# Performance work log

Hardware: AMD Instinct MI355X
Metric: run time of the kernel (lower is better)

## Reference

```python
import jax, jax.numpy as jnp
import numpy as np
import math

B, N, H = 2, 2048, 256
NUM_HEADS, HEAD_DIM = 8, 32
WIN = 32            # window_size
WIN_LEN = 2 * WIN + 1


def setup_inputs() -> dict:
    key = jax.random.key(0)
    ks = jax.random.split(key, 12)
    s = 0.02
    return {
        "x": jax.random.normal(ks[0], (B, N, 4, H), dtype=jnp.float32),
        "Wq": jax.random.normal(ks[1], (H, H), dtype=jnp.float32) * s,
        "bq": jnp.zeros((H,), jnp.float32),
        "Wk": jax.random.normal(ks[2], (H, H), dtype=jnp.float32) * s,
        "bk": jnp.zeros((H,), jnp.float32),
        "Wv": jax.random.normal(ks[3], (H, H), dtype=jnp.float32) * s,
        "bv": jnp.zeros((H,), jnp.float32),
        "Wo": jax.random.normal(ks[4], (H, 3 * H), dtype=jnp.float32) * s,
        "bo": jnp.zeros((3 * H,), jnp.float32),
        "Wvec": jax.random.normal(ks[5], (H, 2 * H), dtype=jnp.float32) * s,
        "alpha_dot": jnp.float32(1.0),
        "alpha_norm": jnp.float32(1.0),
        "Wg": jax.random.normal(ks[6], (2 * H, H), dtype=jnp.float32) * s,
        "bg": jnp.zeros((H,), jnp.float32),
    }


def reference(x, Wq, bq, Wk, bk, Wv, bv, Wo, bo, Wvec, alpha_dot, alpha_norm, Wg, bg):
    h, d = NUM_HEADS, HEAD_DIM
    scale = 1.0 / math.sqrt(d)

    x_scalar = x[:, :, 0]          # (B,N,H)
    vec = x[:, :, 1:4]             # (B,N,3,H)

    q = (x_scalar @ Wq + bq).reshape(B, N, h, d).transpose(0, 2, 1, 3)  # (B,h,N,d)
    k = (x_scalar @ Wk + bk).reshape(B, N, h, d).transpose(0, 2, 1, 3)
    v = (x_scalar @ Wv + bv).reshape(B, N, h, d).transpose(0, 2, 1, 3)

    vec_proj = vec @ Wvec                                # (B,N,3,2H)
    vec1, vec2 = vec_proj[..., :H], vec_proj[..., H:]
    vec_dot = (vec1 * vec2).sum(axis=-2)                 # (B,N,H)
    vec_norm = jnp.linalg.norm(vec, axis=2)              # (B,N,H)

    # (B,N,3,h,d) -> (B,h,N,3*d)
    vec_flat = vec.reshape(B, N, 3, h, d).transpose(0, 3, 1, 2, 4).reshape(B, h, N, 3 * d)

    # sliding-window attention via padded gather (matches torch unfold semantics)
    BH = B * h
    q_l = q.reshape(BH, N, d)
    k_l = k.reshape(BH, N, d)
    v_l = v.reshape(BH, N, d)
    vec_l = vec_flat.reshape(BH, N, 3 * d)

    pad = ((0, 0), (WIN, WIN), (0, 0))
    k_p = jnp.pad(k_l, pad)
    v_p = jnp.pad(v_l, pad)
    vec_p = jnp.pad(vec_l, pad)

    idx = jnp.arange(N)[:, None] + jnp.arange(WIN_LEN)[None, :]  # (N,WIN_LEN)
    k_win = k_p[:, idx]        # (BH,N,WIN_LEN,d)
    v_win = v_p[:, idx]
    vec_win = vec_p[:, idx]    # (BH,N,WIN_LEN,3d)

    attn_scores = jnp.einsum('bid,biwd->biw', q_l, k_win) * scale
    attn_weights = jax.nn.softmax(attn_scores, axis=-1)  # (BH,N,WIN_LEN)

    x_agg = jnp.einsum('biw,biwd->bid', attn_weights, v_win).reshape(B, h, N, d)
    vec_aggr = jnp.einsum('biw,biwd->bid', attn_weights, vec_win).reshape(B, h, N, 3 * d)

    x_out = x_agg.transpose(0, 2, 1, 3).reshape(B, N, H)
    vec_aggr = vec_aggr.reshape(B, h, N, 3, d).transpose(0, 2, 3, 1, 4).reshape(B, N, 3, H)

    invariants = jnp.concatenate([alpha_dot * vec_dot, alpha_norm * vec_norm], axis=-1)
    gate = jax.nn.sigmoid(invariants @ Wg + bg)[:, :, None, :]   # (B,N,1,H)
    vec_combined = gate * vec_aggr + vec                          # gated add mixing

    o = x_out @ Wo + bo
    o1, o2, o3 = o[..., :H], o[..., H:2 * H], o[..., 2 * H:]
    x_updated = vec_dot * o1 + vec_norm * o2 + o3

    x_final = jnp.concatenate([x_updated[:, :, None], vec_combined], axis=2)  # (B,N,4,H)
    return x_final, attn_weights
```

## Files before the change

kernel.cpp:

```cpp
#include <hip/hip_runtime.h>
#include <hip/hip_bf16.h>
#include <math.h>

#define Bc 2
#define Nn 2048
#define Hh 256
#define NH 8
#define Dd 32
#define WIN 32
#define WL 65
#define BN (Bc * Nn)

typedef __attribute__((ext_vector_type(8))) short bf16x8;
typedef __attribute__((ext_vector_type(4))) short s16x4;
typedef __attribute__((ext_vector_type(4))) float f32x4;

__device__ inline short f2bf(float f) {
    union { float f; unsigned u; } v; v.f = f;
    unsigned r = v.u + 0x7fffu + ((v.u >> 16) & 1u);
    return (short)(r >> 16);
}

__device__ inline bf16x8 cvt8(float4 a, float4 b) {
    union { __hip_bfloat162 h[4]; bf16x8 v; } u;
    u.h[0] = __float22bfloat162_rn(make_float2(a.x, a.y));
    u.h[1] = __float22bfloat162_rn(make_float2(a.z, a.w));
    u.h[2] = __float22bfloat162_rn(make_float2(b.x, b.y));
    u.h[3] = __float22bfloat162_rn(make_float2(b.z, b.w));
    return u.v;
}

__global__ __launch_bounds__(256) void prep_kernel(
    const float* __restrict__ x, const float* __restrict__ alpha_norm,
    const float* __restrict__ Wq, const float* __restrict__ Wk, const float* __restrict__ Wv,
    const float* __restrict__ Wvec, const float* __restrict__ Wg, const float* __restrict__ Wo,
    float* __restrict__ vec_norm, short* __restrict__ inv_bf,
    short* __restrict__ WqkvT, short* __restrict__ WvecT,
    short* __restrict__ WgT, short* __restrict__ WoT) {
    __shared__ float Ts[32][33];
    const int t = threadIdx.x;
    if (blockIdx.x >= 640) {
        const int gid = (blockIdx.x - 640) * 256 + t;
        const int bn = gid >> 6, c4 = gid & 63;
        const size_t base = (size_t)bn * 1024 + c4 * 4;
        const float4 v0 = *(const float4*)&x[base + 256];
        const float4 v1 = *(const float4*)&x[base + 512];
        const float4 v2 = *(const float4*)&x[base + 768];
        float4 nr;
        nr.x = sqrtf(v0.x * v0.x + v1.x * v1.x + v2.x * v2.x);
        nr.y = sqrtf(v0.y * v0.y + v1.y * v1.y + v2.y * v2.y);
        nr.z = sqrtf(v0.z * v0.z + v1.z * v1.z + v2.z * v2.z);
        nr.w = sqrtf(v0.w * v0.w + v1.w * v1.w + v2.w * v2.w);
        *(float4*)&vec_norm[(size_t)bn * 256 + c4 * 4] = nr;
        const float an = alpha_norm[0];
        s16x4 iv;
        iv[0] = f2bf(an * nr.x); iv[1] = f2bf(an * nr.y);
        iv[2] = f2bf(an * nr.z); iv[3] = f2bf(an * nr.w);
        *(s16x4*)&inv_bf[(size_t)bn * 512 + 256 + c4 * 4] = iv;
        return;
    }
    const int cc = t & 31, r0 = t >> 5;
    const int id = blockIdx.x;
    const float* W; int ldw; short* WT; int ldwt; int n0s, k0, n0d;
    if (id < 192) {
        const int tn = id >> 3, tk = id & 7, sel = tn >> 3;
        W = sel == 0 ? Wq : (sel == 1 ? Wk : Wv); ldw = 256;
        n0s = (tn & 7) * 32; k0 = tk * 32; WT = WqkvT; ldwt = 256; n0d = tn * 32;
    } else if (id < 320) {
        const int id2 = id - 192, tn = id2 >> 3, tk = id2 & 7;
        W = Wvec; ldw = 512; n0s = tn * 32; k0 = tk * 32; WT = WvecT; ldwt = 256; n0d = n0s;
    } else if (id < 448) {
        const int id3 = id - 320, tn = id3 >> 4, tk = id3 & 15;
        W = Wg; ldw = 256; n0s = tn * 32; k0 = tk * 32; WT = WgT; ldwt = 512; n0d = n0s;
    } else {
        const int id4 = id - 448, tn = id4 >> 3, tk = id4 & 7;
        W = Wo; ldw = 768; n0s = tn * 32; k0 = tk * 32; WT = WoT; ldwt = 256; n0d = n0s;
    }
#pragma unroll
    for (int p = 0; p < 4; ++p) {
        const int rr = r0 + p * 8;
        Ts[rr][cc] = W[(size_t)(k0 + rr) * ldw + n0s + cc];
    }
    __syncthreads();
#pragma unroll
    for (int p = 0; p < 4; ++p) {
        const int rr = r0 + p * 8;
        WT[(size_t)(n0d + rr) * ldwt + k0 + cc] = f2bf(Ts[cc][rr]);
    }
}

__global__ __launch_bounds__(256) void mid_kernel(
    const float* __restrict__ x,
    const short* __restrict__ WqkvT, const short* __restrict__ WvecT,
    const float* __restrict__ bq, const float* __restrict__ bk, const float* __restrict__ bv,
    const float* __restrict__ alpha_dot,
    short* __restrict__ Qb, short* __restrict__ Kb, short* __restrict__ Vb,
    float* __restrict__ vec_dot, short* __restrict__ inv_bf) {
    __shared__ __align__(16) short lds[10240];
    const int bid = blockIdx.x;
    const int t = threadIdx.x, lane = t & 63, wid = t >> 6;
    const int wm = wid & 1, wn = wid >> 1, quad = lane >> 4, lm = lane & 15;
    const int srow = t >> 2, scg = (t & 3) * 8;

    if (bid < 384) {
        short* As = lds;
        short* Bs = lds + 2560;
        const int row0 = (bid & 63) * 64, col0 = (bid >> 6) * 128;
        f32x4 acc[2][4];
#pragma unroll
        for (int mt = 0; mt < 2; ++mt)
#pragma unroll
            for (int nt = 0; nt < 4; ++nt) {
                f32x4 z = {0.f, 0.f, 0.f, 0.f};
                acc[mt][nt] = z;
            }
        float4 pa0 = *(const float4*)&x[(size_t)(row0 + srow) * 1024 + scg];
        float4 pa1 = *(const float4*)&x[(size_t)(row0 + srow) * 1024 + scg + 4];
        bf16x8 pb[2];
#pragma unroll
        for (int p = 0; p < 2; ++p) {
            const int idx = t + p * 256;
            pb[p] = *(const bf16x8*)&WqkvT[(size_t)(col0 + (idx >> 2)) * 256 + (idx & 3) * 8];
        }
        for (int k0 = 0; k0 < 256; k0 += 32) {
            *(bf16x8*)&As[srow * 40 + scg] = cvt8(pa0, pa1);
#pragma unroll
            for (int p = 0; p < 2; ++p) {
                const int idx = t + p * 256;
                *(bf16x8*)&Bs[(idx >> 2) * 40 + (idx & 3) * 8] = pb[p];
            }
            __syncthreads();
            if (k0 + 32 < 256) {
                pa0 = *(const float4*)&x[(size_t)(row0 + srow) * 1024 + k0 + 32 + scg];
                pa1 = *(const float4*)&x[(size_t)(row0 + srow) * 1024 + k0 + 32 + scg + 4];
#pragma unroll
                for (int p = 0; p < 2; ++p) {
                    const int idx = t + p * 256;
                    pb[p] = *(const bf16x8*)&WqkvT[(size_t)(col0 + (idx >> 2)) * 256 + k0 + 32 + (idx & 3) * 8];
                }
            }
            bf16x8 af[2], bfr[4];
#pragma unroll
            for (int mt = 0; mt < 2; ++mt)
                af[mt] = *(bf16x8*)&As[(wm * 32 + mt * 16 + lm) * 40 + quad * 8];
#pragma unroll
            for (int nt = 0; nt < 4; ++nt)
                bfr[nt] = *(bf16x8*)&Bs[(wn * 64 + nt * 16 + lm) * 40 + quad * 8];
#pragma unroll
            for (int mt = 0; mt < 2; ++mt)
#pragma unroll
                for (int nt = 0; nt < 4; ++nt)
                    acc[mt][nt] = __builtin_amdgcn_mfma_f32_16x16x32_bf16(
                        af[mt], bfr[nt], acc[mt][nt], 0, 0, 0);
            __syncthreads();
        }
        const int chunk = col0 >> 8;
        short* dst = chunk == 0 ? Qb : (chunk == 1 ? Kb : Vb);
        const float* bias = chunk == 0 ? bq : (chunk == 1 ? bk : bv);
#pragma unroll
        for (int mt = 0; mt < 2; ++mt)
#pragma unroll
            for (int nt = 0; nt < 4; ++nt) {
                const int cm = (col0 + wn * 64 + nt * 16 + lm) & 255;
                const float bb = bias[cm];
#pragma unroll
                for (int r = 0; r < 4; ++r) {
                    const int row = row0 + wm * 32 + mt * 16 + quad * 4 + r;
                    dst[(size_t)row * 256 + cm] = f2bf(acc[mt][nt][r] + bb);
                }
            }
        return;
    }

    short* As = lds;
    short* Bs = lds + 7680;
    const int vb = bid - 384;
    const int row0 = (vb >> 3) * 64, ch0 = (vb & 7) * 32;
    const int bh_ = t >> 7, bc = (t >> 2) & 31, bcg = (t & 3) * 8;
    f32x4 acc[3][2][2];
#pragma unroll
    for (int p = 0; p < 3; ++p)
#pragma unroll
        for (int h = 0; h < 2; ++h)
#pragma unroll
            for (int mt = 0; mt < 2; ++mt) {
                f32x4 z = {0.f, 0.f, 0.f, 0.f};
                acc[p][h][mt] = z;
            }
    float4 pa0[3], pa1[3];
#pragma unroll
    for (int p = 0; p < 3; ++p) {
        pa0[p] = *(const float4*)&x[(size_t)(row0 + srow) * 1024 + (1 + p) * 256 + scg];
        pa1[p] = *(const float4*)&x[(size_t)(row0 + srow) * 1024 + (1 + p) * 256 + scg + 4];
    }
    bf16x8 pb = *(const bf16x8*)&WvecT[(size_t)(bh_ * 256 + ch0 + bc) * 256 + bcg];
    for (int k0 = 0; k0 < 256; k0 += 32) {
#pragma unroll
        for (int p = 0; p < 3; ++p)
            *(bf16x8*)&As[p * 2560 + srow * 40 + scg] = cvt8(pa0[p], pa1[p]);
        *(bf16x8*)&Bs[bh_ * 1280 + bc * 40 + bcg] = pb;
        __syncthreads();
        if (k0 + 32 < 256) {
#pragma unroll
            for (int p = 0; p < 3; ++p) {
                pa0[p] = *(const float4*)&x[(size_t)(row0 + srow) * 1024 + (1 + p) * 256 + k0 + 32 + scg];
                pa1[p] = *(const float4*)&x[(size_t)(row0 + srow) * 1024 + (1 + p) * 256 + k0 + 32 + scg + 4];
            }
            pb = *(const bf16x8*)&WvecT[(size_t)(bh_ * 256 + ch0 + bc) * 256 + k0 + 32 + bcg];
        }
        bf16x8 af[3][2], bfr[2];
#pragma unroll
        for (int p = 0; p < 3; ++p)
#pragma unroll
            for (int mt = 0; mt < 2; ++mt)
                af[p][mt] = *(bf16x8*)&As[p * 2560 + (wm * 32 + mt * 16 + lm) * 40 + quad * 8];
#pragma unroll
        for (int h = 0; h < 2; ++h)
            bfr[h] = *(bf16x8*)&Bs[h * 1280 + (wn * 16 + lm) * 40 + quad * 8];
#pragma unroll
        for (int p = 0; p < 3; ++p)
#pragma unroll
            for (int h = 0; h < 2; ++h)
#pragma unroll
                for (int mt = 0; mt < 2; ++mt)
                    acc[p][h][mt] = __builtin_amdgcn_mfma_f32_16x16x32_bf16(
                        af[p][mt], bfr[h], acc[p][h][mt], 0, 0, 0);
        __syncthreads();
    }
    const float ad = alpha_dot[0];
#pragma unroll
    for (int mt = 0; mt < 2; ++mt) {
        const int col = ch0 + wn * 16 + lm;
#pragma unroll
        for (int r = 0; r < 4; ++r) {
            const int row = row0 + wm * 32 + mt * 16 + quad * 4 + r;
            float dot = 0.f;
#pragma unroll
            for (int p = 0; p < 3; ++p)
                dot = fmaf(acc[p][0][mt][r], acc[p][1][mt][r], dot);
            vec_dot[(size_t)row * 256 + col] = dot;
            inv_bf[(size_t)row * 512 + col] = f2bf(ad * dot);
        }
    }
}

__global__ __launch_bounds__(256) void gate_attn_kernel(
    const short* __restrict__ inv_bf, const short* __restrict__ WgT,
    const float* __restrict__ bg,
    const short* __restrict__ Qb, const short* __restrict__ Kb,
    const short* __restrict__ Vb, const float* __restrict__ x,
    float* __restrict__ gate, float* __restrict__ attnw,
    float* __restrict__ vec_aggr, short* __restrict__ xout_bf) {
    __shared__ __align__(16) short lds[21760];
    const int bid = blockIdx.x;
    const int t = threadIdx.x, lane = t & 63, wid = t >> 6;
    const int wm = wid & 1, wn = wid >> 1, quad = lane >> 4, lm = lane & 15;

    if (bid < 256) {
        short* As = lds;
        short* Bs = lds + 2560;
        const int row0 = (bid & 63) * 64, col0 = (bid >> 6) * 64;
        const int srow = t >> 2, scg = (t & 3) * 8;
        f32x4 acc[2][2];
#pragma unroll
        for (int mt = 0; mt < 2; ++mt)
#pragma unroll
            for (int nt = 0; nt < 2; ++nt) {
                f32x4 z = {0.f, 0.f, 0.f, 0.f};
                acc[mt][nt] = z;
            }
        bf16x8 pa = *(const bf16x8*)&inv_bf[(size_t)(row0 + srow) * 512 + scg];
        bf16x8 pb = *(const bf16x8*)&WgT[(size_t)(col0 + srow) * 512 + scg];
        for (int k0 = 0; k0 < 512; k0 += 32) {
            *(bf16x8*)&As[srow * 40 + scg] = pa;
            *(bf16x8*)&Bs[srow * 40 + scg] = pb;
            __syncthreads();
            if (k0 + 32 < 512) {
                pa = *(const bf16x8*)&inv_bf[(size_t)(row0 + srow) * 512 + k0 + 32 + scg];
                pb = *(const bf16x8*)&WgT[(size_t)(col0 + srow) * 512 + k0 + 32 + scg];
            }
            bf16x8 af[2], bfr[2];
#pragma unroll
            for (int mt = 0; mt < 2; ++mt)
                af[mt] = *(bf16x8*)&As[(wm * 32 + mt * 16 + lm) * 40 + quad * 8];
#pragma unroll
            for (int nt = 0; nt < 2; ++nt)
                bfr[nt] = *(bf16x8*)&Bs[(wn * 32 + nt * 16 + lm) * 40 + quad * 8];
#pragma unroll
            for (int mt = 0; mt < 2; ++mt)
#pragma unroll
                for (int nt = 0; nt < 2; ++nt)
                    acc[mt][nt] = __builtin_amdgcn_mfma_f32_16x16x32_bf16(
                        af[mt], bfr[nt], acc[mt][nt], 0, 0, 0);
            __syncthreads();
        }
#pragma unroll
        for (int mt = 0; mt < 2; ++mt)
#pragma unroll
            for (int nt = 0; nt < 2; ++nt) {
                const int col = col0 + wn * 32 + nt * 16 + lm;
                const float bb = bg[col];
#pragma unroll
                for (int r = 0; r < 4; ++r) {
                    const int row = row0 + wm * 32 + mt * 16 + quad * 4 + r;
                    const float z = acc[mt][nt][r] + bb;
                    gate[(size_t)row * 256 + col] = 1.f / (1.f + __expf(-z));
                }
            }
        return;
    }

    short* Qs = lds;
    short* Ks = lds + 1280;
    short* Pb = lds + 5120;
    short* St = lds + 8448;
    const int ab = bid - 256;
    const int bh = ab >> 6, tile = ab & 63;
    const int b = bh >> 3, hd = bh & 7;
    const int i0 = tile * 32;

    for (int idx = t; idx < 32 * 104 / 2; idx += 256) ((int*)Pb)[idx] = 0;
    if (t < 128) {
        const int row = t >> 2, cg = t & 3;
        *(bf16x8*)&Qs[row * 40 + cg * 8] =
            *(const bf16x8*)&Qb[((size_t)(b * Nn + i0 + row)) * 256 + hd * 32 + cg * 8];
    }
#pragma unroll
    for (int kk = 0; kk < 2; ++kk) {
        const int idx = t + kk * 256;
        if (idx < 384) {
            const int row = idx >> 2, cg = idx & 3;
            const int j = i0 - WIN + row;
            bf16x8 kv = {0, 0, 0, 0, 0, 0, 0, 0};
            if (j >= 0 && j < Nn)
                kv = *(const bf16x8*)&Kb[((size_t)(b * Nn + j)) * 256 + hd * 32 + cg * 8];
            *(bf16x8*)&Ks[row * 40 + cg * 8] = kv;
        }
    }
    __syncthreads();

    if (wid < 2) {
        const int il0 = wid * 16;
        const bf16x8 aq = *(bf16x8*)&Qs[(il0 + lm) * 40 + quad * 8];
        f32x4 c[6];
#pragma unroll
        for (int nt = 0; nt < 6; ++nt) {
            const bf16x8 bk = *(bf16x8*)&Ks[(nt * 16 + lm) * 40 + quad * 8];
            f32x4 z = {0.f, 0.f, 0.f, 0.f};
            c[nt] = __builtin_amdgcn_mfma_f32_16x16x32_bf16(aq, bk, z, 0, 0, 0);
        }
        float mx[4] = {-1e30f, -1e30f, -1e30f, -1e30f};
#pragma unroll
        for (int nt = 0; nt < 6; ++nt)
#pragma unroll
            for (int r = 0; r < 4; ++r) {
                const int il = il0 + quad * 4 + r;
                const int w = nt * 16 + lm - il;
                const float v = (w >= 0 && w <= 64)
                    ? c[nt][r] * 0.17677669529663687f : -1e30f;
                c[nt][r] = v;
                mx[r] = fmaxf(mx[r], v);
            }
#pragma unroll
        for (int off = 1; off < 16; off <<= 1)
#pragma unroll
            for (int r = 0; r < 4; ++r) mx[r] = fmaxf(mx[r], __shfl_xor(mx[r], off, 64));
        float sm[4] = {0.f, 0.f, 0.f, 0.f};
#pragma unroll
        for (int nt = 0; nt < 6; ++nt)
#pragma unroll
            for (int r = 0; r < 4; ++r) {
                const int il = il0 + quad * 4 + r;
                const int w = nt * 16 + lm - il;
                const float e = (w >= 0 && w <= 64) ? __expf(c[nt][r] - mx[r]) : 0.f;
                c[nt][r] = e;
                sm[r] += e;
            }
#pragma unroll
        for (int off = 1; off < 16; off <<= 1)
#pragma unroll
            for (int r = 0; r < 4; ++r) sm[r] += __shfl_xor(sm[r], off, 64);
        float inv[4];
#pragma unroll
        for (int r = 0; r < 4; ++r) inv[r] = 1.f / sm[r];
#pragma unroll
        for (int nt = 0; nt < 6; ++nt)
#pragma unroll
            for (int r = 0; r < 4; ++r) {
                const int il = il0 + quad * 4 + r;
                const int jr = nt * 16 + lm;
                const int w = jr - il;
                if (w >= 0 && w <= 64) {
                    const float pw = c[nt][r] * inv[r];
                    attnw[((size_t)bh * Nn + (i0 + il)) * WL + w] = pw;
                    Pb[il * 104 + jr] = f2bf(pw);
                }
            }
    } else {
        const int tt = t - 128;
        const int chunk = tt >> 3, j0 = tt & 7;
#pragma unroll
        for (int it = 0; it < 12; ++it) {
            const int jr = j0 + it * 8;
            const int j = i0 - WIN + jr;
            bf16x8 val = {0, 0, 0, 0, 0, 0, 0, 0};
            if (j >= 0 && j < Nn) {
                if (chunk < 4) {
                    val = *(const bf16x8*)&Vb[((size_t)(b * Nn + j)) * 256 + hd * 32 + chunk * 8];
                } else {
                    const int vc = (chunk - 4) >> 2, d0 = ((chunk - 4) & 3) * 8;
                    const float* src = &x[((size_t)(b * Nn + j)) * 1024 + (1 + vc) * 256 + hd * 32 + d0];
                    val = cvt8(*(const float4*)src, *(const float4*)(src + 4));
                }
            }
#pragma unroll
            for (int u = 0; u < 8; ++u) St[(chunk * 8 + u) * 104 + jr] = val[u];
        }
    }
    __syncthreads();

    f32x4 acc[4];
#pragma unroll
    for (int nt = 0; nt < 4; ++nt) {
        f32x4 z = {0.f, 0.f, 0.f, 0.f};
        acc[nt] = z;
    }
#pragma unroll
    for (int ks = 0; ks < 3; ++ks) {
        const bf16x8 ap = *(bf16x8*)&Pb[(wm * 16 + lm) * 104 + ks * 32 + quad * 8];
#pragma unroll
        for (int nt = 0; nt < 4; ++nt) {
            const bf16x8 bs = *(bf16x8*)&St[(wn * 64 + nt * 16 + lm) * 104 + ks * 32 + quad * 8];
            acc[nt] = __builtin_amdgcn_mfma_f32_16x16x32_bf16(ap, bs, acc[nt], 0, 0, 0);
        }
    }
#pragma unroll
    for (int nt = 0; nt < 4; ++nt) {
        const int dim = wn * 64 + nt * 16 + lm;
#pragma unroll
        for (int r = 0; r < 4; ++r) {
            const int i = wm * 16 + quad * 4 + r;
            const size_t bn = (size_t)(b * Nn + i0 + i);
            if (dim < 32) {
                xout_bf[bn * 256 + hd * 32 + dim] = f2bf(acc[nt][r]);
            } else {
                const int dm = dim - 32, c = dm >> 5, dd = dm & 31;
                vec_aggr[((size_t)c * BN + bn) * 256 + hd * 32 + dd] = acc[nt][r];
            }
        }
    }
}

__global__ __launch_bounds__(256) void out_kernel(
    const short* __restrict__ A, const short* __restrict__ BT,
    const float* __restrict__ bo,
    const float* __restrict__ vec_dot, const float* __restrict__ vec_norm,
    const float* __restrict__ gate, const float* __restrict__ vec_aggr,
    const float* __restrict__ x, float* __restrict__ out) {
    __shared__ short As[64 * 40];
    __shared__ short Bs[3][64 * 40];
    const int row0 = (blockIdx.x & 63) * 64, ch0 = (blockIdx.x >> 6) * 64;
    const int t = threadIdx.x, lane = t & 63, wid = t >> 6;
    const int wm = wid & 1, wn = wid >> 1, quad = lane >> 4, lm = lane & 15;
    const int srow = t >> 2, scg = (t & 3) * 8;
    f32x4 acc[3][2][2];
#pragma unroll
    for (int p = 0; p < 3; ++p)
#pragma unroll
        for (int mt = 0; mt < 2; ++mt)
#pragma unroll
            for (int nt = 0; nt < 2; ++nt) {
                f32x4 z = {0.f, 0.f, 0.f, 0.f};
                acc[p][mt][nt] = z;
            }
    bf16x8 pa, pb[3];
    pa = *(const bf16x8*)&A[(size_t)(row0 + srow) * 256 + scg];
#pragma unroll
    for (int p = 0; p < 3; ++p)
        pb[p] = *(const bf16x8*)&BT[(size_t)(p * 256 + ch0 + srow) * 256 + scg];
    for (int k0 = 0; k0 < 256; k0 += 32) {
        *(bf16x8*)&As[srow * 40 + scg] = pa;
#pragma unroll
        for (int p = 0; p < 3; ++p)
            *(bf16x8*)&Bs[p][srow * 40 + scg] = pb[p];
        __syncthreads();
        if (k0 + 32 < 256) {
            pa = *(const bf16x8*)&A[(size_t)(row0 + srow) * 256 + k0 + 32 + scg];
#pragma unroll
            for (int p = 0; p < 3; ++p)
                pb[p] = *(const bf16x8*)&BT[(size_t)(p * 256 + ch0 + srow) * 256 + k0 + 32 + scg];
        }
        bf16x8 af[2], bfr[3][2];
#pragma unroll
        for (int mt = 0; mt < 2; ++mt)
            af[mt] = *(bf16x8*)&As[(wm * 32 + mt * 16 + lm) * 40 + quad * 8];
#pragma unroll
        for (int p = 0; p < 3; ++p)
#pragma unroll
            for (int nt = 0; nt < 2; ++nt)
                bfr[p][nt] = *(bf16x8*)&Bs[p][(wn * 32 + nt * 16 + lm) * 40 + quad * 8];
#pragma unroll
        for (int p = 0; p < 3; ++p)
#pragma unroll
            for (int mt = 0; mt < 2; ++mt)
#pragma unroll
                for (int nt = 0; nt < 2; ++nt)
                    acc[p][mt][nt] = __builtin_amdgcn_mfma_f32_16x16x32_bf16(
                        af[mt], bfr[p][nt], acc[p][mt][nt], 0, 0, 0);
        __syncthreads();
    }
#pragma unroll
    for (int mt = 0; mt < 2; ++mt)
#pragma unroll
        for (int nt = 0; nt < 2; ++nt) {
            const int col = ch0 + wn * 32 + nt * 16 + lm;
            const float b1 = bo[col], b2 = bo[256 + col], b3 = bo[512 + col];
#pragma unroll
            for (int r = 0; r < 4; ++r) {
                const int row = row0 + wm * 32 + mt * 16 + quad * 4 + r;
                const float o1 = acc[0][mt][nt][r] + b1;
                const float o2 = acc[1][mt][nt][r] + b2;
                const float o3 = acc[2][mt][nt][r] + b3;
                const float vd = vec_dot[(size_t)row * 256 + col];
                const float vn = vec_norm[(size_t)row * 256 + col];
                out[(size_t)row * 1024 + col] = vd * o1 + vn * o2 + o3;
            }
        }
#pragma unroll
    for (int c = 0; c < 3; ++c) {
#pragma unroll
        for (int it = 0; it < 4; ++it) {
            const int idx = t + it * 256;
            const int row = row0 + (idx >> 4), col = ch0 + (idx & 15) * 4;
            const float4 g4 = *(const float4*)&gate[(size_t)row * 256 + col];
            const float4 va = *(const float4*)&vec_aggr[((size_t)c * BN + row) * 256 + col];
            const float4 xv = *(const float4*)&x[(size_t)row * 1024 + (1 + c) * 256 + col];
            float4 o;
            o.x = fmaf(g4.x, va.x, xv.x);
            o.y = fmaf(g4.y, va.y, xv.y);
            o.z = fmaf(g4.z, va.z, xv.z);
            o.w = fmaf(g4.w, va.w, xv.w);
            *(float4*)&out[(size_t)row * 1024 + (1 + c) * 256 + col] = o;
        }
    }
}

extern "C" void kernel_launch(void* const* d_in, const int* in_sizes, int n_in,
                              void* d_out, int out_size, void* d_ws, size_t ws_size,
                              hipStream_t stream) {
    const float* x  = (const float*)d_in[0];
    const float* Wq = (const float*)d_in[1];
    const float* bq = (const float*)d_in[2];
    const float* Wk = (const float*)d_in[3];
    const float* bk = (const float*)d_in[4];
    const float* Wv = (const float*)d_in[5];
    const float* bv = (const float*)d_in[6];
    const float* Wo = (const float*)d_in[7];
    const float* bo = (const float*)d_in[8];
    const float* Wvec = (const float*)d_in[9];
    const float* alpha_dot  = (const float*)d_in[10];
    const float* alpha_norm = (const float*)d_in[11];
    const float* Wg = (const float*)d_in[12];
    const float* bg = (const float*)d_in[13];

    float* ws = (float*)d_ws;
    float* vec_dot  = ws;
    float* vec_norm = ws + 1048576;
    float* gate     = ws + 2097152;
    float* vec_aggr = ws + 3145728;
    short* sb = (short*)(ws + 6291456);
    short* xout_bf = sb;
    short* Q_bf    = sb + 1048576;
    short* K_bf    = sb + 2097152;
    short* V_bf    = sb + 3145728;
    short* inv_bf  = sb + 4194304;
    short* WqkvT   = sb + 6291456;
    short* WvecT   = sb + 6488064;
    short* WgT     = sb + 6619136;
    short* WoT     = sb + 6750208;

    float* out = (float*)d_out;
    float* attnw = out + (size_t)Bc * Nn * 4 * Hh;

    prep_kernel<<<1664, 256, 0, stream>>>(x, alpha_norm, Wq, Wk, Wv, Wvec, Wg, Wo,
                                          vec_norm, inv_bf, WqkvT, WvecT, WgT, WoT);
    mid_kernel<<<896, 256, 0, stream>>>(x, WqkvT, WvecT, bq, bk, bv, alpha_dot,
                                        Q_bf, K_bf, V_bf, vec_dot, inv_bf);
    gate_attn_kernel<<<1280, 256, 0, stream>>>(inv_bf, WgT, bg, Q_bf, K_bf, V_bf, x,
                                               gate, attnw, vec_aggr, xout_bf);
    out_kernel<<<256, 256, 0, stream>>>(xout_bf, WoT, bo, vec_dot, vec_norm,
                                        gate, vec_aggr, x, out);
}
```

Baseline: 157.4 us.

## Pre-cast x to bf16 once, store vec_aggr in bf16, retile vec-proj and out GEMMs

A first pass converts the scalar and vector channels of x to bf16 buffers, and those are reused by the QKV GEMM, the Wvec GEMM and the attention gather instead of re-reading and converting fp32 x each time. The intermediate vec_aggr is stored as bf16 to halve its write and read traffic. The Wvec GEMM is retiled to 16-row blocks that keep all three vector components and the full K dimension in LDS, and out_kernel uses 32-row tiles to launch twice as many blocks. The cost is an extra elementwise pass with more bf16 writes, a larger LDS footprint, and bf16 rounding of vec_aggr before the gated add.

```diff
diff --git a/kernel.cpp b/kernel.cpp
--- a/kernel.cpp
+++ b/kernel.cpp
@@ -20,7 +20,11 @@
     unsigned r = v.u + 0x7fffu + ((v.u >> 16) & 1u);
     return (short)(r >> 16);
 }
-
+__device__ inline float bf2f(short s) {
+    union { float f; unsigned u; } v;
+    v.u = ((unsigned)(unsigned short)s) << 16;
+    return v.f;
+}
 __device__ inline bf16x8 cvt8(float4 a, float4 b) {
     union { __hip_bfloat162 h[4]; bf16x8 v; } u;
     u.h[0] = __float22bfloat162_rn(make_float2(a.x, a.y));
@@ -30,37 +34,33 @@
     return u.v;
 }
 
-__global__ __launch_bounds__(256) void prep_kernel(
+__global__ __launch_bounds__(256) void castxw_kernel(
     const float* __restrict__ x, const float* __restrict__ alpha_norm,
     const float* __restrict__ Wq, const float* __restrict__ Wk, const float* __restrict__ Wv,
     const float* __restrict__ Wvec, const float* __restrict__ Wg, const float* __restrict__ Wo,
+    short* __restrict__ xs_bf, short* __restrict__ vec_bf,
     float* __restrict__ vec_norm, short* __restrict__ inv_bf,
     short* __restrict__ WqkvT, short* __restrict__ WvecT,
     short* __restrict__ WgT, short* __restrict__ WoT) {
     __shared__ float Ts[32][33];
+    if (blockIdx.x < 4096) {
+        const int idx = blockIdx.x * 256 + threadIdx.x;
+        const int bn = idx >> 8, ch = idx & 255;
+        const size_t base = (size_t)bn * 1024 + ch;
+        const float xs = x[base];
+        const float v0 = x[base + 256], v1 = x[base + 512], v2 = x[base + 768];
+        xs_bf[(size_t)bn * 256 + ch] = f2bf(xs);
+        vec_bf[((size_t)0 * BN + bn) * 256 + ch] = f2bf(v0);
+        vec_bf[((size_t)1 * BN + bn) * 256 + ch] = f2bf(v1);
+        vec_bf[((size_t)2 * BN + bn) * 256 + ch] = f2bf(v2);
+        const float nrm = sqrtf(v0 * v0 + v1 * v1 + v2 * v2);
+        vec_norm[(size_t)bn * 256 + ch] = nrm;
+        inv_bf[(size_t)bn * 512 + 256 + ch] = f2bf(alpha_norm[0] * nrm);
+        return;
+    }
     const int t = threadIdx.x;
-    if (blockIdx.x >= 640) {
-        const int gid = (blockIdx.x - 640) * 256 + t;
-        const int bn = gid >> 6, c4 = gid & 63;
-        const size_t base = (size_t)bn * 1024 + c4 * 4;
-        const float4 v0 = *(const float4*)&x[base + 256];
-        const float4 v1 = *(const float4*)&x[base + 512];
-        const float4 v2 = *(const float4*)&x[base + 768];
-        float4 nr;
-        nr.x = sqrtf(v0.x * v0.x + v1.x * v1.x + v2.x * v2.x);
-        nr.y = sqrtf(v0.y * v0.y + v1.y * v1.y + v2.y * v2.y);
-        nr.z = sqrtf(v0.z * v0.z + v1.z * v1.z + v2.z * v2.z);
-        nr.w = sqrtf(v0.w * v0.w + v1.w * v1.w + v2.w * v2.w);
-        *(float4*)&vec_norm[(size_t)bn * 256 + c4 * 4] = nr;
-        const float an = alpha_norm[0];
-        s16x4 iv;
-        iv[0] = f2bf(an * nr.x); iv[1] = f2bf(an * nr.y);
-        iv[2] = f2bf(an * nr.z); iv[3] = f2bf(an * nr.w);
-        *(s16x4*)&inv_bf[(size_t)bn * 512 + 256 + c4 * 4] = iv;
-        return;
-    }
     const int cc = t & 31, r0 = t >> 5;
-    const int id = blockIdx.x;
+    const int id = blockIdx.x - 4096;
     const float* W; int ldw; short* WT; int ldwt; int n0s, k0, n0d;
     if (id < 192) {
         const int tn = id >> 3, tk = id & 7, sel = tn >> 3;
@@ -89,23 +89,24 @@
     }
 }
 
-__global__ __launch_bounds__(256) void mid_kernel(
-    const float* __restrict__ x,
+__global__ __launch_bounds__(256) void fused_mid(
+    const short* __restrict__ xs_bf, const short* __restrict__ vec_bf,
     const short* __restrict__ WqkvT, const short* __restrict__ WvecT,
     const float* __restrict__ bq, const float* __restrict__ bk, const float* __restrict__ bv,
     const float* __restrict__ alpha_dot,
     short* __restrict__ Qb, short* __restrict__ Kb, short* __restrict__ Vb,
     float* __restrict__ vec_dot, short* __restrict__ inv_bf) {
-    __shared__ __align__(16) short lds[10240];
+    __shared__ __align__(16) short lds[22912];
     const int bid = blockIdx.x;
     const int t = threadIdx.x, lane = t & 63, wid = t >> 6;
-    const int wm = wid & 1, wn = wid >> 1, quad = lane >> 4, lm = lane & 15;
-    const int srow = t >> 2, scg = (t & 3) * 8;
+    const int quad = lane >> 4, lm = lane & 15;
 
     if (bid < 384) {
         short* As = lds;
         short* Bs = lds + 2560;
         const int row0 = (bid & 63) * 64, col0 = (bid >> 6) * 128;
+        const int wm = wid & 1, wn = wid >> 1;
+        const int srow = t >> 2, scg = (t & 3) * 8;
         f32x4 acc[2][4];
 #pragma unroll
         for (int mt = 0; mt < 2; ++mt)
@@ -114,8 +115,7 @@
                 f32x4 z = {0.f, 0.f, 0.f, 0.f};
                 acc[mt][nt] = z;
             }
-        float4 pa0 = *(const float4*)&x[(size_t)(row0 + srow) * 1024 + scg];
-        float4 pa1 = *(const float4*)&x[(size_t)(row0 + srow) * 1024 + scg + 4];
+        bf16x8 pa = *(const bf16x8*)&xs_bf[(size_t)(row0 + srow) * 256 + scg];
         bf16x8 pb[2];
 #pragma unroll
         for (int p = 0; p < 2; ++p) {
@@ -123,7 +123,7 @@
             pb[p] = *(const bf16x8*)&WqkvT[(size_t)(col0 + (idx >> 2)) * 256 + (idx & 3) * 8];
         }
         for (int k0 = 0; k0 < 256; k0 += 32) {
-            *(bf16x8*)&As[srow * 40 + scg] = cvt8(pa0, pa1);
+            *(bf16x8*)&As[srow * 40 + scg] = pa;
 #pragma unroll
             for (int p = 0; p < 2; ++p) {
                 const int idx = t + p * 256;
@@ -131,8 +131,7 @@
             }
             __syncthreads();
             if (k0 + 32 < 256) {
-                pa0 = *(const float4*)&x[(size_t)(row0 + srow) * 1024 + k0 + 32 + scg];
-                pa1 = *(const float4*)&x[(size_t)(row0 + srow) * 1024 + k0 + 32 + scg + 4];
+                pa = *(const bf16x8*)&xs_bf[(size_t)(row0 + srow) * 256 + k0 + 32 + scg];
 #pragma unroll
                 for (int p = 0; p < 2; ++p) {
                     const int idx = t + p * 256;
@@ -173,71 +172,81 @@
     }
 
     short* As = lds;
-    short* Bs = lds + 7680;
+    short* Bs = lds + 12672;
     const int vb = bid - 384;
-    const int row0 = (vb >> 3) * 64, ch0 = (vb & 7) * 32;
-    const int bh_ = t >> 7, bc = (t >> 2) & 31, bcg = (t & 3) * 8;
+    const int row0 = (vb >> 1) * 16, ch0 = (vb & 1) * 128;
+
+#pragma unroll
+    for (int q = 0; q < 6; ++q) {
+        const int idx = t + q * 256;
+        const int p = idx >> 9, rem = idx & 511, row = rem >> 5, kg = rem & 31;
+        *(bf16x8*)&As[(p * 16 + row) * 264 + kg * 8] =
+            *(const bf16x8*)&vec_bf[((size_t)p * BN + row0 + row) * 256 + kg * 8];
+    }
     f32x4 acc[3][2][2];
 #pragma unroll
     for (int p = 0; p < 3; ++p)
 #pragma unroll
         for (int h = 0; h < 2; ++h)
 #pragma unroll
-            for (int mt = 0; mt < 2; ++mt) {
+            for (int nt = 0; nt < 2; ++nt) {
                 f32x4 z = {0.f, 0.f, 0.f, 0.f};
-                acc[p][h][mt] = z;
-            }
-    float4 pa0[3], pa1[3];
-#pragma unroll
-    for (int p = 0; p < 3; ++p) {
-        pa0[p] = *(const float4*)&x[(size_t)(row0 + srow) * 1024 + (1 + p) * 256 + scg];
-        pa1[p] = *(const float4*)&x[(size_t)(row0 + srow) * 1024 + (1 + p) * 256 + scg + 4];
-    }
-    bf16x8 pb = *(const bf16x8*)&WvecT[(size_t)(bh_ * 256 + ch0 + bc) * 256 + bcg];
+                acc[p][h][nt] = z;
+            }
+    bf16x8 pb[4];
+#pragma unroll
+    for (int q = 0; q < 4; ++q) {
+        const int idx = t + q * 256;
+        const int h = idx >> 9, rem = idx & 511, c = rem >> 2, kg = rem & 3;
+        pb[q] = *(const bf16x8*)&WvecT[(size_t)(h * 256 + ch0 + c) * 256 + kg * 8];
+    }
+    __syncthreads();
     for (int k0 = 0; k0 < 256; k0 += 32) {
 #pragma unroll
-        for (int p = 0; p < 3; ++p)
-            *(bf16x8*)&As[p * 2560 + srow * 40 + scg] = cvt8(pa0[p], pa1[p]);
-        *(bf16x8*)&Bs[bh_ * 1280 + bc * 40 + bcg] = pb;
+        for (int q = 0; q < 4; ++q) {
+            const int idx = t + q * 256;
+            const int h = idx >> 9, rem = idx & 511, c = rem >> 2, kg = rem & 3;
+            *(bf16x8*)&Bs[(h * 128 + c) * 40 + kg * 8] = pb[q];
+        }
         __syncthreads();
         if (k0 + 32 < 256) {
 #pragma unroll
-            for (int p = 0; p < 3; ++p) {
-                pa0[p] = *(const float4*)&x[(size_t)(row0 + srow) * 1024 + (1 + p) * 256 + k0 + 32 + scg];
-                pa1[p] = *(const float4*)&x[(size_t)(row0 + srow) * 1024 + (1 + p) * 256 + k0 + 32 + scg + 4];
-            }
-            pb = *(const bf16x8*)&WvecT[(size_t)(bh_ * 256 + ch0 + bc) * 256 + k0 + 32 + bcg];
-        }
-        bf16x8 af[3][2], bfr[2];
+            for (int q = 0; q < 4; ++q) {
+                const int idx = t + q * 256;
+                const int h = idx >> 9, rem = idx & 511, c = rem >> 2, kg = rem & 3;
+                pb[q] = *(const bf16x8*)&WvecT[(size_t)(h * 256 + ch0 + c) * 256 + k0 + 32 + kg * 8];
+            }
+        }
+        bf16x8 af[3], bfr[2][2];
 #pragma unroll
         for (int p = 0; p < 3; ++p)
-#pragma unroll
-            for (int mt = 0; mt < 2; ++mt)
-                af[p][mt] = *(bf16x8*)&As[p * 2560 + (wm * 32 + mt * 16 + lm) * 40 + quad * 8];
+            af[p] = *(bf16x8*)&As[(p * 16 + lm) * 264 + k0 + quad * 8];
 #pragma unroll
         for (int h = 0; h < 2; ++h)
-            bfr[h] = *(bf16x8*)&Bs[h * 1280 + (wn * 16 + lm) * 40 + quad * 8];
+#pragma unroll
+            for (int nt = 0; nt < 2; ++nt)
+                bfr[h][nt] = *(bf16x8*)&Bs[(h * 128 + wid * 32 + nt * 16 + lm) * 40 + quad * 8];
 #pragma unroll
         for (int p = 0; p < 3; ++p)
 #pragma unroll
             for (int h = 0; h < 2; ++h)
 #pragma unroll
-                for (int mt = 0; mt < 2; ++mt)
-                    acc[p][h][mt] = __builtin_amdgcn_mfma_f32_16x16x32_bf16(
-                        af[p][mt], bfr[h], acc[p][h][mt], 0, 0, 0);
+                for (int nt = 0; nt < 2; ++nt)
+                    acc[p][h][nt] = __builtin_amdgcn_mfma_f32_16x16x32_bf16(
+                        af[p], bfr[h][nt], acc[p][h][nt], 0, 0, 0);
         __syncthreads();
     }
     const float ad = alpha_dot[0];
 #pragma unroll
-    for (int mt = 0; mt < 2; ++mt) {
-        const int col = ch0 + wn * 16 + lm;
+    for (int nt = 0; nt < 2; ++nt) {
+        const int col = ch0 + wid * 32 + nt * 16 + lm;
 #pragma unroll
         for (int r = 0; r < 4; ++r) {
-            const int row = row0 + wm * 32 + mt * 16 + quad * 4 + r;
+            const int row = row0 + quad * 4 + r;
             float dot = 0.f;
 #pragma unroll
             for (int p = 0; p < 3; ++p)
-                dot = fmaf(acc[p][0][mt][r], acc[p][1][mt][r], dot);
+                dot = fmaf(acc[p][0][nt][r], acc[p][1][nt][r], dot);
             vec_dot[(size_t)row * 256 + col] = dot;
             inv_bf[(size_t)row * 512 + col] = f2bf(ad * dot);
         }
@@ -248,9 +257,9 @@
     const short* __restrict__ inv_bf, const short* __restrict__ WgT,
     const float* __restrict__ bg,
     const short* __restrict__ Qb, const short* __restrict__ Kb,
-    const short* __restrict__ Vb, const float* __restrict__ x,
+    const short* __restrict__ Vb, const short* __restrict__ vec_bf,
     float* __restrict__ gate, float* __restrict__ attnw,
-    float* __restrict__ vec_aggr, short* __restrict__ xout_bf) {
+    short* __restrict__ vec_aggr_bf, short* __restrict__ xout_bf) {
     __shared__ __align__(16) short lds[21760];
     const int bid = blockIdx.x;
     const int t = threadIdx.x, lane = t & 63, wid = t >> 6;
@@ -409,8 +418,7 @@
                     val = *(const bf16x8*)&Vb[((size_t)(b * Nn + j)) * 256 + hd * 32 + chunk * 8];
                 } else {
                     const int vc = (chunk - 4) >> 2, d0 = ((chunk - 4) & 3) * 8;
-                    const float* src = &x[((size_t)(b * Nn + j)) * 1024 + (1 + vc) * 256 + hd * 32 + d0];
-                    val = cvt8(*(const float4*)src, *(const float4*)(src + 4));
+                    val = *(const bf16x8*)&vec_bf[((size_t)vc * BN + b * Nn + j) * 256 + hd * 32 + d0];
                 }
             }
 #pragma unroll
@@ -445,7 +453,7 @@
                 xout_bf[bn * 256 + hd * 32 + dim] = f2bf(acc[nt][r]);
             } else {
                 const int dm = dim - 32, c = dm >> 5, dd = dm & 31;
-                vec_aggr[((size_t)c * BN + bn) * 256 + hd * 32 + dd] = acc[nt][r];
+                vec_aggr_bf[((size_t)c * BN + bn) * 256 + hd * 32 + dd] = f2bf(acc[nt][r]);
             }
         }
     }
@@ -455,45 +463,51 @@
     const short* __restrict__ A, const short* __restrict__ BT,
     const float* __restrict__ bo,
     const float* __restrict__ vec_dot, const float* __restrict__ vec_norm,
-    const float* __restrict__ gate, const float* __restrict__ vec_aggr,
+    const float* __restrict__ gate, const short* __restrict__ vec_aggr_bf,
     const float* __restrict__ x, float* __restrict__ out) {
-    __shared__ short As[64 * 40];
-    __shared__ short Bs[3][64 * 40];
-    const int row0 = (blockIdx.x & 63) * 64, ch0 = (blockIdx.x >> 6) * 64;
+    __shared__ __align__(16) short As[32 * 40];
+    __shared__ __align__(16) short Bs[3][64 * 40];
+    const int row0 = (blockIdx.x & 127) * 32, ch0 = (blockIdx.x >> 7) * 64;
     const int t = threadIdx.x, lane = t & 63, wid = t >> 6;
     const int wm = wid & 1, wn = wid >> 1, quad = lane >> 4, lm = lane & 15;
-    const int srow = t >> 2, scg = (t & 3) * 8;
-    f32x4 acc[3][2][2];
+    f32x4 acc[3][2];
 #pragma unroll
     for (int p = 0; p < 3; ++p)
 #pragma unroll
-        for (int mt = 0; mt < 2; ++mt)
-#pragma unroll
-            for (int nt = 0; nt < 2; ++nt) {
-                f32x4 z = {0.f, 0.f, 0.f, 0.f};
-                acc[p][mt][nt] = z;
-            }
-    bf16x8 pa, pb[3];
-    pa = *(const bf16x8*)&A[(size_t)(row0 + srow) * 256 + scg];
-#pragma unroll
-    for (int p = 0; p < 3; ++p)
-        pb[p] = *(const bf16x8*)&BT[(size_t)(p * 256 + ch0 + srow) * 256 + scg];
+        for (int nt = 0; nt < 2; ++nt) {
+            f32x4 z = {0.f, 0.f, 0.f, 0.f};
+            acc[p][nt] = z;
+        }
+    bf16x8 pa = {0, 0, 0, 0, 0, 0, 0, 0};
+    const int arow = t >> 2, acg = (t & 3) * 8;
+    if (t < 128) pa = *(const bf16x8*)&A[(size_t)(row0 + arow) * 256 + acg];
+    bf16x8 pb[3];
+#pragma unroll
+    for (int q = 0; q < 3; ++q) {
+        const int idx = t + q * 256;
+        const int p = idx >> 8, rem = idx & 255, brow = rem >> 2, bkg = (rem & 3) * 8;
+        pb[q] = *(const bf16x8*)&BT[(size_t)(p * 256 + ch0 + brow) * 256 + bkg];
+    }
     for (int k0 = 0; k0 < 256; k0 += 32) {
-        *(bf16x8*)&As[srow * 40 + scg] = pa;
-#pragma unroll
-        for (int p = 0; p < 3; ++p)
-            *(bf16x8*)&Bs[p][srow * 40 + scg] = pb[p];
+        if (t < 128) *(bf16x8*)&As[arow * 40 + acg] = pa;
+#pragma unroll
+        for (int q = 0; q < 3; ++q) {
+            const int idx = t + q * 256;
+            const int p = idx >> 8, rem = idx & 255, brow = rem >> 2, bkg = (rem & 3) * 8;
+            *(bf16x8*)&Bs[p][brow * 40 + bkg] = pb[q];
+        }
         __syncthreads();
         if (k0 + 32 < 256) {
-            pa = *(const bf16x8*)&A[(size_t)(row0 + srow) * 256 + k0 + 32 + scg];
-#pragma unroll
-            for (int p = 0; p < 3; ++p)
-                pb[p] = *(const bf16x8*)&BT[(size_t)(p * 256 + ch0 + srow) * 256 + k0 + 32 + scg];
-        }
-        bf16x8 af[2], bfr[3][2];
-#pragma unroll
-        for (int mt = 0; mt < 2; ++mt)
-            af[mt] = *(bf16x8*)&As[(wm * 32 + mt * 16 + lm) * 40 + quad * 8];
+            if (t < 128) pa = *(const bf16x8*)&A[(size_t)(row0 + arow) * 256 + k0 + 32 + acg];
+#pragma unroll
+            for (int q = 0; q < 3; ++q) {
+                const int idx = t + q * 256;
+                const int p = idx >> 8, rem = idx & 255, brow = rem >> 2, bkg = (rem & 3) * 8;
+                pb[q] = *(const bf16x8*)&BT[(size_t)(p * 256 + ch0 + brow) * 256 + k0 + 32 + bkg];
+            }
+        }
+        const bf16x8 af = *(bf16x8*)&As[(wm * 16 + lm) * 40 + quad * 8];
+        bf16x8 bfr[3][2];
 #pragma unroll
         for (int p = 0; p < 3; ++p)
 #pragma unroll
@@ -502,44 +516,40 @@
 #pragma unroll
         for (int p = 0; p < 3; ++p)
 #pragma unroll
-            for (int mt = 0; mt < 2; ++mt)
-#pragma unroll
-                for (int nt = 0; nt < 2; ++nt)
-                    acc[p][mt][nt] = __builtin_amdgcn_mfma_f32_16x16x32_bf16(
-                        af[mt], bfr[p][nt], acc[p][mt][nt], 0, 0, 0);
+            for (int nt = 0; nt < 2; ++nt)
+                acc[p][nt] = __builtin_amdgcn_mfma_f32_16x16x32_bf16(
+                    af, bfr[p][nt], acc[p][nt], 0, 0, 0);
         __syncthreads();
     }
 #pragma unroll
-    for (int mt = 0; mt < 2; ++mt)
-#pragma unroll
-        for (int nt = 0; nt < 2; ++nt) {
-            const int col = ch0 + wn * 32 + nt * 16 + lm;
-            const float b1 = bo[col], b2 = bo[256 + col], b3 = bo[512 + col];
-#pragma unroll
-            for (int r = 0; r < 4; ++r) {
-                const int row = row0 + wm * 32 + mt * 16 + quad * 4 + r;
-                const float o1 = acc[0][mt][nt][r] + b1;
-                const float o2 = acc[1][mt][nt][r] + b2;
-                const float o3 = acc[2][mt][nt][r] + b3;
-                const float vd = vec_dot[(size_t)row * 256 + col];
-                const float vn = vec_norm[(size_t)row * 256 + col];
-                out[(size_t)row * 1024 + col] = vd * o1 + vn * o2 + o3;
-            }
-        }
+    for (int nt = 0; nt < 2; ++nt) {
+        const int col = ch0 + wn * 32 + nt * 16 + lm;
+        const float b1 = bo[col], b2 = bo[256 + col], b3 = bo[512 + col];
+#pragma unroll
+        for (int r = 0; r < 4; ++r) {
+            const int row = row0 + wm * 16 + quad * 4 + r;
+            const float o1 = acc[0][nt][r] + b1;
+            const float o2 = acc[1][nt][r] + b2;
+            const float o3 = acc[2][nt][r] + b3;
+            const float vd = vec_dot[(size_t)row * 256 + col];
+            const float vn = vec_norm[(size_t)row * 256 + col];
+            out[(size_t)row * 1024 + col] = vd * o1 + vn * o2 + o3;
+        }
+    }
 #pragma unroll
     for (int c = 0; c < 3; ++c) {
 #pragma unroll
-        for (int it = 0; it < 4; ++it) {
+        for (int it = 0; it < 2; ++it) {
             const int idx = t + it * 256;
             const int row = row0 + (idx >> 4), col = ch0 + (idx & 15) * 4;
             const float4 g4 = *(const float4*)&gate[(size_t)row * 256 + col];
-            const float4 va = *(const float4*)&vec_aggr[((size_t)c * BN + row) * 256 + col];
+            const s16x4 va = *(const s16x4*)&vec_aggr_bf[((size_t)c * BN + row) * 256 + col];
             const float4 xv = *(const float4*)&x[(size_t)row * 1024 + (1 + c) * 256 + col];
             float4 o;
-            o.x = fmaf(g4.x, va.x, xv.x);
-            o.y = fmaf(g4.y, va.y, xv.y);
-            o.z = fmaf(g4.z, va.z, xv.z);
-            o.w = fmaf(g4.w, va.w, xv.w);
+            o.x = fmaf(g4.x, bf2f(va[0]), xv.x);
+            o.y = fmaf(g4.y, bf2f(va[1]), xv.y);
+            o.z = fmaf(g4.z, bf2f(va[2]), xv.z);
+            o.w = fmaf(g4.w, bf2f(va[3]), xv.w);
             *(float4*)&out[(size_t)row * 1024 + (1 + c) * 256 + col] = o;
         }
     }
@@ -567,27 +577,30 @@
     float* vec_dot  = ws;
     float* vec_norm = ws + 1048576;
     float* gate     = ws + 2097152;
-    float* vec_aggr = ws + 3145728;
-    short* sb = (short*)(ws + 6291456);
-    short* xout_bf = sb;
-    short* Q_bf    = sb + 1048576;
-    short* K_bf    = sb + 2097152;
-    short* V_bf    = sb + 3145728;
-    short* inv_bf  = sb + 4194304;
-    short* WqkvT   = sb + 6291456;
-    short* WvecT   = sb + 6488064;
-    short* WgT     = sb + 6619136;
-    short* WoT     = sb + 6750208;
+    short* sb = (short*)(ws + 3145728);
+    short* xs_bf       = sb;
+    short* vec_bf      = sb + 1048576;
+    short* inv_bf      = sb + 4194304;
+    short* xout_bf     = sb + 6291456;
+    short* Q_bf        = sb + 7340032;
+    short* K_bf        = sb + 8388608;
+    short* V_bf        = sb + 9437184;
+    short* vec_aggr_bf = sb + 10485760;
+    short* WqkvT       = sb + 13631488;
+    short* WvecT       = sb + 13828096;
+    short* WgT         = sb + 13959168;
+    short* WoT         = sb + 14090240;
 
     float* out = (float*)d_out;
     float* attnw = out + (size_t)Bc * Nn * 4 * Hh;
 
-    prep_kernel<<<1664, 256, 0, stream>>>(x, alpha_norm, Wq, Wk, Wv, Wvec, Wg, Wo,
-                                          vec_norm, inv_bf, WqkvT, WvecT, WgT, WoT);
-    mid_kernel<<<896, 256, 0, stream>>>(x, WqkvT, WvecT, bq, bk, bv, alpha_dot,
-                                        Q_bf, K_bf, V_bf, vec_dot, inv_bf);
-    gate_attn_kernel<<<1280, 256, 0, stream>>>(inv_bf, WgT, bg, Q_bf, K_bf, V_bf, x,
-                                               gate, attnw, vec_aggr, xout_bf);
-    out_kernel<<<256, 256, 0, stream>>>(xout_bf, WoT, bo, vec_dot, vec_norm,
-                                        gate, vec_aggr, x, out);
-}
+    castxw_kernel<<<4736, 256, 0, stream>>>(x, alpha_norm, Wq, Wk, Wv, Wvec, Wg, Wo,
+                                            xs_bf, vec_bf, vec_norm, inv_bf,
+                                            WqkvT, WvecT, WgT, WoT);
+    fused_mid<<<896, 256, 0, stream>>>(xs_bf, vec_bf, WqkvT, WvecT, bq, bk, bv,
+                                       alpha_dot, Q_bf, K_bf, V_bf, vec_dot, inv_bf);
+    gate_attn_kernel<<<1280, 256, 0, stream>>>(inv_bf, WgT, bg, Q_bf, K_bf, V_bf,
+                                               vec_bf, gate, attnw, vec_aggr_bf, xout_bf);
+    out_kernel<<<512, 256, 0, stream>>>(xout_bf, WoT, bo, vec_dot, vec_norm,
+                                        gate, vec_aggr_bf, x, out);
+}
```

After: 137.5 us. 1.14x faster.
